# Performance work log

Hardware: AMD Instinct MI355X
Metric: run time of the kernel (lower is better)

## Reference

```python
import jax, jax.numpy as jnp
import numpy as np

TOP_K = 10
RANKING_WEIGHT = 0.3
UP_WEIGHT = 1.0
DOWN_WEIGHT = 0.5
NEG = 1e9  # finite stand-in for -inf so softmax/grads stay NaN-free


def setup_inputs() -> dict:
    key = jax.random.key(0)
    k1, k2, k3, k4 = jax.random.split(key, 4)
    B, N = 1024, 5000
    up_logits = jax.random.normal(k1, (B, N), jnp.float32)
    down_logits = jax.random.normal(k2, (B, N), jnp.float32)
    y_true = jax.random.normal(k3, (B, N), jnp.float32) * 0.05  # daily returns
    masks = jax.random.randint(k4, (B, N), 0, 2).astype(jnp.int32)
    return {"up_logits": up_logits, "down_logits": down_logits,
            "y_true": y_true, "masks": masks}


def _bce_with_logits(x, z):
    # softplus(x) - x*z  ==  -[z*log(sig(x)) + (1-z)*log(1-sig(x))]
    return jax.nn.softplus(x) - x * z


def reference(up_logits, down_logits, y_true, masks):
    maskb = masks > 0                                   # [B, N]
    maskf = maskb.astype(up_logits.dtype)
    num_valid = maskf.sum(-1)                           # [B]
    nv_safe = jnp.maximum(num_valid, 1.0)
    k = jnp.minimum(TOP_K, num_valid.astype(jnp.int32))  # [B] min(top_k, num)

    # Descending rank of y_true among valid entries (invalid pushed to bottom).
    y_desc = jnp.where(maskb, y_true, -NEG)
    rank_desc = jnp.argsort(jnp.argsort(-y_desc, axis=-1), axis=-1)  # [B, N]
    up_labels = (rank_desc < k[:, None]).astype(up_logits.dtype)

    # Ascending rank (biggest losers) for down path.
    y_asc = jnp.where(maskb, y_true, NEG)
    rank_asc = jnp.argsort(jnp.argsort(y_asc, axis=-1), axis=-1)
    down_labels = (rank_asc < k[:, None]).astype(down_logits.dtype)

    # Mean BCE over valid entries per row.
    up_loss = jnp.sum(_bce_with_logits(up_logits, up_labels) * maskf, -1) / nv_safe
    down_loss = jnp.sum(_bce_with_logits(down_logits, down_labels) * maskf, -1) / nv_safe

    # Listwise KL: softmax over valid entries; kl_div(log p, q, 'batchmean')
    # with 1D input of size num divides the sum by num.
    logp = jax.nn.log_softmax(jnp.where(maskb, up_logits, -NEG), axis=-1)
    logq = jax.nn.log_softmax(jnp.where(maskb, y_true, -NEG), axis=-1)
    q = jnp.exp(logq)
    kl = jnp.sum(jnp.where(maskb, q * (logq - logp), 0.0), -1) / nv_safe

    batch_loss = UP_WEIGHT * up_loss + DOWN_WEIGHT * down_loss + RANKING_WEIGHT * kl
    batch_loss = jnp.where(num_valid > 0, batch_loss, 0.0)  # skip empty rows
    return jnp.sum(batch_loss) / up_logits.shape[0]
```

## Files before the change

kernel.cpp:

```cpp
#include <hip/hip_runtime.h>
#include <math.h>

#define NCOLS 5000
#define NF4   1250
#define BLOCK 256
#define NWAVES (BLOCK / 64)
#define NITER 5
#define TOPKK 10
#define TR    3
#define CAP 128

__device__ __forceinline__ unsigned mono_f32(float f) {
  unsigned u = __float_as_uint(f);
  return (u & 0x80000000u) ? ~u : (u | 0x80000000u);
}

__device__ __forceinline__ float wave_sum_f(float v) {
#pragma unroll
  for (int o = 1; o < 64; o <<= 1) v += __shfl_xor(v, o);
  return v;
}
__device__ __forceinline__ int wave_sum_i(int v) {
#pragma unroll
  for (int o = 1; o < 64; o <<= 1) v += __shfl_xor(v, o);
  return v;
}
__device__ __forceinline__ unsigned wave_max_u(unsigned v) {
#pragma unroll
  for (int o = 1; o < 64; o <<= 1) {
    unsigned w = __shfl_xor(v, o);
    v = w > v ? w : v;
  }
  return v;
}

extern "C" __global__ __launch_bounds__(BLOCK, 4)
void row_loss_kernel(const float* __restrict__ up, const float* __restrict__ down,
                     const float* __restrict__ yt, const int* __restrict__ masks,
                     float* __restrict__ ws, float* __restrict__ out,
                     float inv_nrows, int use_ws) {
  __shared__ uint4 km_s[NITER * BLOCK];
  __shared__ float red_f[6][NWAVES];
  __shared__ int red_i[NWAVES];
  __shared__ unsigned t1w_t[NWAVES];
  __shared__ unsigned t1w_b[NWAVES];
  __shared__ unsigned keys_t[CAP];
  __shared__ int      col_t[CAP];
  __shared__ unsigned keys_b[CAP];
  __shared__ int      col_b[CAP];
  __shared__ int ct, cb;
  __shared__ float s_res[2];

  const int tid = threadIdx.x;
  const int lane = tid & 63;
  const int wv = tid >> 6;
  const int row = blockIdx.x;
  const long long b4 = (long long)row * NF4;
  const long long base = (long long)row * NCOLS;

  const float4* up4 = (const float4*)up + b4;
  const float4* dn4 = (const float4*)down + b4;
  const float4* yt4 = (const float4*)yt + b4;
  const int4*   mk4 = (const int4*)masks + b4;

  if (tid == 0) { ct = 0; cb = 0; }

  float4 y4[NITER], u4[NITER], d4[NITER];
  int4 m4[NITER];
#pragma unroll
  for (int j = 0; j < NITER; ++j) {
    const int f = j * BLOCK + tid;
    const int fc = f < NF4 ? f : NF4 - 1;
    y4[j] = yt4[fc];
    u4[j] = up4[fc];
    d4[j] = dn4[fc];
    m4[j] = mk4[fc];
  }
  __builtin_amdgcn_sched_barrier(0);

  int nv_l = 0;
  float sq = 0.f, sp = 0.f, seyy = 0.f, seyu = 0.f, aspu = 0.f, aspd = 0.f;
  unsigned tmax = 0u, tbmax = 0u;
#pragma unroll
  for (int j = 0; j < NITER; ++j) {
    const bool inb = (j * BLOCK + tid) < NF4;
    const float* yp = (const float*)&y4[j];
    const float* upp = (const float*)&u4[j];
    const float* dp = (const float*)&d4[j];
    const int* mp = (const int*)&m4[j];
    unsigned kk[4];
#pragma unroll
    for (int c = 0; c < 4; ++c) {
      const bool valid = inb && (mp[c] > 0);
      const float y = yp[c], u = upp[c], d = dp[c];
      const unsigned kd = valid ? mono_f32(y) : 0u;
      const unsigned kb = valid ? ~kd : 0u;
      kk[c] = kd;
      tmax = kd > tmax ? kd : tmax;
      tbmax = kb > tbmax ? kb : tbmax;
      if (valid) {
        nv_l++;
        const float ey = __expf(y);
        const float eu = __expf(u);
        const float ed = __expf(d);
        sq += ey;
        seyy += ey * y;
        seyu += ey * u;
        sp += eu;
        aspu += (u > 15.f) ? u : __logf(1.f + eu);
        aspd += (d > 15.f) ? d : __logf(1.f + ed);
      }
    }
    km_s[j * BLOCK + tid] = make_uint4(kk[0], kk[1], kk[2], kk[3]);
  }

  nv_l = wave_sum_i(nv_l);
  sq = wave_sum_f(sq);
  sp = wave_sum_f(sp);
  seyy = wave_sum_f(seyy);
  seyu = wave_sum_f(seyu);
  aspu = wave_sum_f(aspu);
  aspd = wave_sum_f(aspd);
  if (lane == 0) {
    red_i[wv] = nv_l;
    red_f[0][wv] = sq;  red_f[1][wv] = sp;
    red_f[2][wv] = seyy; red_f[3][wv] = seyu;
    red_f[4][wv] = aspu; red_f[5][wv] = aspd;
  }

  {
    unsigned vt = tmax, vb = tbmax, t1t = 0u, t1b = 0u;
#pragma unroll
    for (int r = 0; r < TR; ++r) {
      unsigned mt = wave_max_u(vt);
      unsigned mb = wave_max_u(vb);
      if (vt == mt) vt = 0u;
      if (vb == mb) vb = 0u;
      t1t = mt; t1b = mb;
    }
    if (lane == 0) { t1w_t[wv] = t1t; t1w_b[wv] = t1b; }
  }
  __syncthreads();

  int nv = 0;
#pragma unroll
  for (int w = 0; w < NWAVES; ++w) nv += red_i[w];
  const int k = nv < TOPKK ? nv : TOPKK;

  unsigned t1 = 0xFFFFFFFFu, t1b = 0xFFFFFFFFu;
#pragma unroll
  for (int w = 0; w < NWAVES; ++w) {
    t1 = t1w_t[w] < t1 ? t1w_t[w] : t1;
    t1b = t1w_b[w] < t1b ? t1w_b[w] : t1b;
  }

#pragma unroll
  for (int j = 0; j < NITER; ++j) {
    const uint4 kk4 = km_s[j * BLOCK + tid];
    const unsigned ka[4] = {kk4.x, kk4.y, kk4.z, kk4.w};
#pragma unroll
    for (int c = 0; c < 4; ++c) {
      const unsigned kd = ka[c];
      if (kd != 0u) {
        const int col = ((j * BLOCK + tid) << 2) + c;
        if (kd >= t1) {
          int i = atomicAdd(&ct, 1);
          if (i < CAP) { keys_t[i] = kd; col_t[i] = col; }
        }
        const unsigned kb = ~kd;
        if (kb >= t1b) {
          int i = atomicAdd(&cb, 1);
          if (i < CAP) { keys_b[i] = kb; col_b[i] = col; }
        }
      }
    }
  }
  __syncthreads();

  if (wv == 0) {
    const int n = ct < CAP ? ct : CAP;
    const unsigned k0 = (lane < n) ? keys_t[lane] : 0u;
    const unsigned k1 = (64 + lane < n) ? keys_t[64 + lane] : 0u;
    unsigned thr = 0u;
#pragma unroll
    for (int b = 31; b >= 0; --b) {
      const unsigned t = thr | (1u << b);
      const int c = __popcll(__ballot(k0 >= t)) + __popcll(__ballot(k1 >= t));
      thr = (c >= k) ? t : thr;
    }
    float su = 0.f;
    if (k0 >= thr && k0 != 0u) su += up[base + col_t[lane]];
    if (k1 >= thr && k1 != 0u) su += up[base + col_t[64 + lane]];
    su = wave_sum_f(su);
    if (lane == 0) s_res[0] = su;
  } else if (wv == 1) {
    const int n = cb < CAP ? cb : CAP;
    const unsigned k0 = (lane < n) ? keys_b[lane] : 0u;
    const unsigned k1 = (64 + lane < n) ? keys_b[64 + lane] : 0u;
    unsigned thr = 0u;
#pragma unroll
    for (int b = 31; b >= 0; --b) {
      const unsigned t = thr | (1u << b);
      const int c = __popcll(__ballot(k0 >= t)) + __popcll(__ballot(k1 >= t));
      thr = (c >= k) ? t : thr;
    }
    float sd = 0.f;
    if (k0 >= thr && k0 != 0u) sd += down[base + col_b[lane]];
    if (k1 >= thr && k1 != 0u) sd += down[base + col_b[64 + lane]];
    sd = wave_sum_f(sd);
    if (lane == 0) s_res[1] = sd;
  }
  __syncthreads();

  if (tid == 0) {
    float loss = 0.f;
    if (nv > 0) {
      float SQ = 0.f, SP = 0.f, SYY = 0.f, SYU = 0.f, ASU = 0.f, ASD = 0.f;
#pragma unroll
      for (int w = 0; w < NWAVES; ++w) {
        SQ += red_f[0][w]; SP += red_f[1][w];
        SYY += red_f[2][w]; SYU += red_f[3][w];
        ASU += red_f[4][w]; ASD += red_f[5][w];
      }
      const float SU = s_res[0];
      const float SD = s_res[1];
      const float kl = (SYY - SYU) / SQ - __logf(SQ) + __logf(SP);
      const float up_loss = ASU - SU;
      const float dn_loss = ASD - SD;
      loss = (up_loss + 0.5f * dn_loss + 0.3f * kl) / (float)nv;
    }
    if (use_ws) {
      ws[row] = loss;
    } else if (loss != 0.f) {
      atomicAdd(out, loss * inv_nrows);
    }
  }
}

extern "C" __global__ __launch_bounds__(256)
void reduce_loss_kernel(const float* __restrict__ ws, float* __restrict__ out,
                        int n, float inv_n) {
  __shared__ float part[4];
  const int tid = threadIdx.x;
  const int lane = tid & 63;
  const int wv = tid >> 6;
  float s = 0.f;
  const int n4 = n >> 2;
  const float4* w4 = (const float4*)ws;
  for (int i = tid; i < n4; i += 256) {
    const float4 v = w4[i];
    s += (v.x + v.y) + (v.z + v.w);
  }
  for (int i = (n4 << 2) + tid; i < n; i += 256) s += ws[i];
  s = wave_sum_f(s);
  if (lane == 0) part[wv] = s;
  __syncthreads();
  if (tid == 0) out[0] = (part[0] + part[1] + part[2] + part[3]) * inv_n;
}

extern "C" void kernel_launch(void* const* d_in, const int* in_sizes, int n_in,
                              void* d_out, int out_size, void* d_ws, size_t ws_size,
                              hipStream_t stream) {
  const float* up_logits   = (const float*)d_in[0];
  const float* down_logits = (const float*)d_in[1];
  const float* y_true      = (const float*)d_in[2];
  const int*   masks       = (const int*)d_in[3];

  const int nrows = in_sizes[0] / NCOLS;
  const int use_ws = (d_ws != nullptr && ws_size >= (size_t)nrows * sizeof(float)) ? 1 : 0;

  hipMemsetAsync(d_out, 0, sizeof(float) * (size_t)out_size, stream);
  row_loss_kernel<<<nrows, BLOCK, 0, stream>>>(up_logits, down_logits, y_true,
                                               masks, (float*)d_ws, (float*)d_out,
                                               1.0f / (float)nrows, use_ws);
  if (use_ws) {
    reduce_loss_kernel<<<1, 256, 0, stream>>>((const float*)d_ws, (float*)d_out,
                                              nrows, 1.0f / (float)nrows);
  }
}
```

Measured before the change: 115.3 us.

## Use 1024-thread blocks per row with single-max wave thresholds and unconditional workspace reduction

Each row is now processed by a 1024-thread block, so each thread loads at most two float4 chunks per input instead of five. The goal is more memory-level parallelism and less per-thread serial work. The top-3 per-wave threshold search becomes a single per-wave max, with the minimum taken over 16 waves and zero-valued waves ignored. Candidate capacity grows to 256 to absorb the looser threshold. The memset and atomic fallback path are removed, so the two-kernel workspace reduction always runs; this assumes the workspace is always provided.

```diff
diff --git a/kernel.cpp b/kernel.cpp
--- a/kernel.cpp
+++ b/kernel.cpp
@@ -3,12 +3,11 @@
 
 #define NCOLS 5000
 #define NF4   1250
-#define BLOCK 256
-#define NWAVES (BLOCK / 64)
-#define NITER 5
+#define BLOCK 1024
+#define NWAVES 16
+#define T2    (NF4 - BLOCK)
 #define TOPKK 10
-#define TR    3
-#define CAP 128
+#define CAP   256
 
 __device__ __forceinline__ unsigned mono_f32(float f) {
   unsigned u = __float_as_uint(f);
@@ -34,20 +33,17 @@
   return v;
 }
 
-extern "C" __global__ __launch_bounds__(BLOCK, 4)
+extern "C" __global__ __launch_bounds__(BLOCK, 8)
 void row_loss_kernel(const float* __restrict__ up, const float* __restrict__ down,
                      const float* __restrict__ yt, const int* __restrict__ masks,
-                     float* __restrict__ ws, float* __restrict__ out,
-                     float inv_nrows, int use_ws) {
-  __shared__ uint4 km_s[NITER * BLOCK];
+                     float* __restrict__ ws) {
+  __shared__ uint4 km_s[NF4];
   __shared__ float red_f[6][NWAVES];
   __shared__ int red_i[NWAVES];
   __shared__ unsigned t1w_t[NWAVES];
   __shared__ unsigned t1w_b[NWAVES];
-  __shared__ unsigned keys_t[CAP];
-  __shared__ int      col_t[CAP];
-  __shared__ unsigned keys_b[CAP];
-  __shared__ int      col_b[CAP];
+  __shared__ unsigned keys_t[CAP]; __shared__ int col_t[CAP];
+  __shared__ unsigned keys_b[CAP]; __shared__ int col_b[CAP];
   __shared__ int ct, cb;
   __shared__ float s_res[2];
 
@@ -58,61 +54,58 @@
   const long long b4 = (long long)row * NF4;
   const long long base = (long long)row * NCOLS;
 
+  if (tid == 0) { ct = 0; cb = 0; }
+
   const float4* up4 = (const float4*)up + b4;
   const float4* dn4 = (const float4*)down + b4;
   const float4* yt4 = (const float4*)yt + b4;
   const int4*   mk4 = (const int4*)masks + b4;
 
-  if (tid == 0) { ct = 0; cb = 0; }
-
-  float4 y4[NITER], u4[NITER], d4[NITER];
-  int4 m4[NITER];
-#pragma unroll
-  for (int j = 0; j < NITER; ++j) {
-    const int f = j * BLOCK + tid;
-    const int fc = f < NF4 ? f : NF4 - 1;
-    y4[j] = yt4[fc];
-    u4[j] = up4[fc];
-    d4[j] = dn4[fc];
-    m4[j] = mk4[fc];
-  }
+  const bool inb2 = tid < T2;
+  const int f2 = inb2 ? BLOCK + tid : NF4 - 1;
+
+  float4 y0 = yt4[tid], u0 = up4[tid], d0 = dn4[tid];
+  int4   m0 = mk4[tid];
+  float4 y1 = yt4[f2],  u1 = up4[f2],  d1 = dn4[f2];
+  int4   m1 = mk4[f2];
   __builtin_amdgcn_sched_barrier(0);
 
   int nv_l = 0;
   float sq = 0.f, sp = 0.f, seyy = 0.f, seyu = 0.f, aspu = 0.f, aspd = 0.f;
   unsigned tmax = 0u, tbmax = 0u;
-#pragma unroll
-  for (int j = 0; j < NITER; ++j) {
-    const bool inb = (j * BLOCK + tid) < NF4;
-    const float* yp = (const float*)&y4[j];
-    const float* upp = (const float*)&u4[j];
-    const float* dp = (const float*)&d4[j];
-    const int* mp = (const int*)&m4[j];
-    unsigned kk[4];
-#pragma unroll
-    for (int c = 0; c < 4; ++c) {
-      const bool valid = inb && (mp[c] > 0);
-      const float y = yp[c], u = upp[c], d = dp[c];
-      const unsigned kd = valid ? mono_f32(y) : 0u;
-      const unsigned kb = valid ? ~kd : 0u;
-      kk[c] = kd;
-      tmax = kd > tmax ? kd : tmax;
-      tbmax = kb > tbmax ? kb : tbmax;
-      if (valid) {
-        nv_l++;
-        const float ey = __expf(y);
-        const float eu = __expf(u);
-        const float ed = __expf(d);
-        sq += ey;
-        seyy += ey * y;
-        seyu += ey * u;
-        sp += eu;
-        aspu += (u > 15.f) ? u : __logf(1.f + eu);
-        aspd += (d > 15.f) ? d : __logf(1.f + ed);
-      }
-    }
-    km_s[j * BLOCK + tid] = make_uint4(kk[0], kk[1], kk[2], kk[3]);
-  }
+  unsigned kk[4];
+
+#define ELEM(idx, Y, U, D, M, INB)                                      \
+  {                                                                     \
+    const bool valid = (INB) && ((M) > 0);                              \
+    const float y = (Y), u = (U), d = (D);                              \
+    const unsigned kd = valid ? mono_f32(y) : 0u;                       \
+    const unsigned kb = valid ? ~kd : 0u;                               \
+    kk[idx] = kd;                                                       \
+    tmax = kd > tmax ? kd : tmax;                                       \
+    tbmax = kb > tbmax ? kb : tbmax;                                    \
+    if (valid) {                                                        \
+      nv_l++;                                                           \
+      const float ey = __expf(y);                                      \
+      const float eu = __expf(u);                                      \
+      const float ed = __expf(d);                                      \
+      sq += ey; seyy += ey * y; seyu += ey * u; sp += eu;               \
+      aspu += (u > 15.f) ? u : __logf(1.f + eu);                       \
+      aspd += (d > 15.f) ? d : __logf(1.f + ed);                       \
+    }                                                                   \
+  }
+
+  ELEM(0, y0.x, u0.x, d0.x, m0.x, true)
+  ELEM(1, y0.y, u0.y, d0.y, m0.y, true)
+  ELEM(2, y0.z, u0.z, d0.z, m0.z, true)
+  ELEM(3, y0.w, u0.w, d0.w, m0.w, true)
+  km_s[tid] = make_uint4(kk[0], kk[1], kk[2], kk[3]);
+  ELEM(0, y1.x, u1.x, d1.x, m1.x, inb2)
+  ELEM(1, y1.y, u1.y, d1.y, m1.y, inb2)
+  ELEM(2, y1.z, u1.z, d1.z, m1.z, inb2)
+  ELEM(3, y1.w, u1.w, d1.w, m1.w, inb2)
+  if (inb2) km_s[BLOCK + tid] = make_uint4(kk[0], kk[1], kk[2], kk[3]);
+#undef ELEM
 
   nv_l = wave_sum_i(nv_l);
   sq = wave_sum_f(sq);
@@ -121,24 +114,15 @@
   seyu = wave_sum_f(seyu);
   aspu = wave_sum_f(aspu);
   aspd = wave_sum_f(aspd);
+  const unsigned wmax_t = wave_max_u(tmax);
+  const unsigned wmax_b = wave_max_u(tbmax);
   if (lane == 0) {
     red_i[wv] = nv_l;
     red_f[0][wv] = sq;  red_f[1][wv] = sp;
     red_f[2][wv] = seyy; red_f[3][wv] = seyu;
     red_f[4][wv] = aspu; red_f[5][wv] = aspd;
-  }
-
-  {
-    unsigned vt = tmax, vb = tbmax, t1t = 0u, t1b = 0u;
-#pragma unroll
-    for (int r = 0; r < TR; ++r) {
-      unsigned mt = wave_max_u(vt);
-      unsigned mb = wave_max_u(vb);
-      if (vt == mt) vt = 0u;
-      if (vb == mb) vb = 0u;
-      t1t = mt; t1b = mb;
-    }
-    if (lane == 0) { t1w_t[wv] = t1t; t1w_b[wv] = t1b; }
+    t1w_t[wv] = wmax_t;
+    t1w_b[wv] = wmax_b;
   }
   __syncthreads();
 
@@ -150,27 +134,45 @@
   unsigned t1 = 0xFFFFFFFFu, t1b = 0xFFFFFFFFu;
 #pragma unroll
   for (int w = 0; w < NWAVES; ++w) {
-    t1 = t1w_t[w] < t1 ? t1w_t[w] : t1;
-    t1b = t1w_b[w] < t1b ? t1w_b[w] : t1b;
-  }
-
-#pragma unroll
-  for (int j = 0; j < NITER; ++j) {
-    const uint4 kk4 = km_s[j * BLOCK + tid];
-    const unsigned ka[4] = {kk4.x, kk4.y, kk4.z, kk4.w};
+    const unsigned a = t1w_t[w], b = t1w_b[w];
+    if (a != 0u && a < t1) t1 = a;
+    if (b != 0u && b < t1b) t1b = b;
+  }
+
+  {
+    const uint4 c0 = km_s[tid];
+    const unsigned ka[4] = {c0.x, c0.y, c0.z, c0.w};
 #pragma unroll
     for (int c = 0; c < 4; ++c) {
       const unsigned kd = ka[c];
       if (kd != 0u) {
-        const int col = ((j * BLOCK + tid) << 2) + c;
         if (kd >= t1) {
           int i = atomicAdd(&ct, 1);
-          if (i < CAP) { keys_t[i] = kd; col_t[i] = col; }
+          if (i < CAP) { keys_t[i] = kd; col_t[i] = (tid << 2) + c; }
         }
         const unsigned kb = ~kd;
         if (kb >= t1b) {
           int i = atomicAdd(&cb, 1);
-          if (i < CAP) { keys_b[i] = kb; col_b[i] = col; }
+          if (i < CAP) { keys_b[i] = kb; col_b[i] = (tid << 2) + c; }
+        }
+      }
+    }
+  }
+  if (inb2) {
+    const uint4 c1 = km_s[BLOCK + tid];
+    const unsigned ka[4] = {c1.x, c1.y, c1.z, c1.w};
+#pragma unroll
+    for (int c = 0; c < 4; ++c) {
+      const unsigned kd = ka[c];
+      if (kd != 0u) {
+        if (kd >= t1) {
+          int i = atomicAdd(&ct, 1);
+          if (i < CAP) { keys_t[i] = kd; col_t[i] = ((BLOCK + tid) << 2) + c; }
+        }
+        const unsigned kb = ~kd;
+        if (kb >= t1b) {
+          int i = atomicAdd(&cb, 1);
+          if (i < CAP) { keys_b[i] = kb; col_b[i] = ((BLOCK + tid) << 2) + c; }
         }
       }
     }
@@ -179,34 +181,44 @@
 
   if (wv == 0) {
     const int n = ct < CAP ? ct : CAP;
-    const unsigned k0 = (lane < n) ? keys_t[lane] : 0u;
-    const unsigned k1 = (64 + lane < n) ? keys_t[64 + lane] : 0u;
+    unsigned kc[4];
+#pragma unroll
+    for (int t = 0; t < 4; ++t)
+      kc[t] = (t * 64 + lane < n) ? keys_t[t * 64 + lane] : 0u;
     unsigned thr = 0u;
 #pragma unroll
     for (int b = 31; b >= 0; --b) {
       const unsigned t = thr | (1u << b);
-      const int c = __popcll(__ballot(k0 >= t)) + __popcll(__ballot(k1 >= t));
+      int c = 0;
+#pragma unroll
+      for (int q = 0; q < 4; ++q) c += __popcll(__ballot(kc[q] >= t));
       thr = (c >= k) ? t : thr;
     }
     float su = 0.f;
-    if (k0 >= thr && k0 != 0u) su += up[base + col_t[lane]];
-    if (k1 >= thr && k1 != 0u) su += up[base + col_t[64 + lane]];
+#pragma unroll
+    for (int t = 0; t < 4; ++t)
+      if (kc[t] >= thr && kc[t] != 0u) su += up[base + col_t[t * 64 + lane]];
     su = wave_sum_f(su);
     if (lane == 0) s_res[0] = su;
   } else if (wv == 1) {
     const int n = cb < CAP ? cb : CAP;
-    const unsigned k0 = (lane < n) ? keys_b[lane] : 0u;
-    const unsigned k1 = (64 + lane < n) ? keys_b[64 + lane] : 0u;
+    unsigned kc[4];
+#pragma unroll
+    for (int t = 0; t < 4; ++t)
+      kc[t] = (t * 64 + lane < n) ? keys_b[t * 64 + lane] : 0u;
     unsigned thr = 0u;
 #pragma unroll
     for (int b = 31; b >= 0; --b) {
       const unsigned t = thr | (1u << b);
-      const int c = __popcll(__ballot(k0 >= t)) + __popcll(__ballot(k1 >= t));
+      int c = 0;
+#pragma unroll
+      for (int q = 0; q < 4; ++q) c += __popcll(__ballot(kc[q] >= t));
       thr = (c >= k) ? t : thr;
     }
     float sd = 0.f;
-    if (k0 >= thr && k0 != 0u) sd += down[base + col_b[lane]];
-    if (k1 >= thr && k1 != 0u) sd += down[base + col_b[64 + lane]];
+#pragma unroll
+    for (int t = 0; t < 4; ++t)
+      if (kc[t] >= thr && kc[t] != 0u) sd += down[base + col_b[t * 64 + lane]];
     sd = wave_sum_f(sd);
     if (lane == 0) s_res[1] = sd;
   }
@@ -229,11 +241,7 @@
       const float dn_loss = ASD - SD;
       loss = (up_loss + 0.5f * dn_loss + 0.3f * kl) / (float)nv;
     }
-    if (use_ws) {
-      ws[row] = loss;
-    } else if (loss != 0.f) {
-      atomicAdd(out, loss * inv_nrows);
-    }
+    ws[row] = loss;
   }
 }
 
@@ -267,14 +275,9 @@
   const int*   masks       = (const int*)d_in[3];
 
   const int nrows = in_sizes[0] / NCOLS;
-  const int use_ws = (d_ws != nullptr && ws_size >= (size_t)nrows * sizeof(float)) ? 1 : 0;
-
-  hipMemsetAsync(d_out, 0, sizeof(float) * (size_t)out_size, stream);
+
   row_loss_kernel<<<nrows, BLOCK, 0, stream>>>(up_logits, down_logits, y_true,
-                                               masks, (float*)d_ws, (float*)d_out,
-                                               1.0f / (float)nrows, use_ws);
-  if (use_ws) {
-    reduce_loss_kernel<<<1, 256, 0, stream>>>((const float*)d_ws, (float*)d_out,
-                                              nrows, 1.0f / (float)nrows);
-  }
-}
+                                               masks, (float*)d_ws);
+  reduce_loss_kernel<<<1, 256, 0, stream>>>((const float*)d_ws, (float*)d_out,
+                                            nrows, 1.0f / (float)nrows);
+}
```

Measured after the change: 119.0 us. 1.03x slower.

## Stream row data into LDS via async global_load_lds with staged waits

Applied to the files above, without the earlier changes.

Loads y_true, up and down rows straight into shared memory using the async global-to-LDS load builtin, and processes each chunk as soon as its loads land, using explicit vmcnt waits. The stored key array is replaced by a per-thread valid bitmask, and keys are recomputed from LDS. The final top-k gather now reads LDS instead of global memory. The atomic/memset fallback path is dropped and the reduce kernel always runs. The cost is much larger LDS use (about 60KB, launch bounds lowered to 2), which reduces occupancy, and correctness depends on hand-counted vmcnt values.

```diff
diff --git a/kernel.cpp b/kernel.cpp
--- a/kernel.cpp
+++ b/kernel.cpp
@@ -3,12 +3,13 @@
 
 #define NCOLS 5000
 #define NF4   1250
+#define NF4P  1280
 #define BLOCK 256
-#define NWAVES (BLOCK / 64)
+#define NWAVES 4
 #define NITER 5
 #define TOPKK 10
 #define TR    3
-#define CAP 128
+#define CAP   128
 
 __device__ __forceinline__ unsigned mono_f32(float f) {
   unsigned u = __float_as_uint(f);
@@ -34,20 +35,25 @@
   return v;
 }
 
-extern "C" __global__ __launch_bounds__(BLOCK, 4)
+__device__ __forceinline__ void gl_lds16(const float4* g, float4* l) {
+  __builtin_amdgcn_global_load_lds(
+      (const __attribute__((address_space(1))) void*)(g),
+      (__attribute__((address_space(3))) void*)(l), 16, 0, 0);
+}
+
+extern "C" __global__ __launch_bounds__(BLOCK, 2)
 void row_loss_kernel(const float* __restrict__ up, const float* __restrict__ down,
                      const float* __restrict__ yt, const int* __restrict__ masks,
-                     float* __restrict__ ws, float* __restrict__ out,
-                     float inv_nrows, int use_ws) {
-  __shared__ uint4 km_s[NITER * BLOCK];
+                     float* __restrict__ ws) {
+  __shared__ float4 y_s[NF4P];
+  __shared__ float4 u_s[NF4P];
+  __shared__ float4 d_s[NF4P];
   __shared__ float red_f[6][NWAVES];
   __shared__ int red_i[NWAVES];
   __shared__ unsigned t1w_t[NWAVES];
   __shared__ unsigned t1w_b[NWAVES];
-  __shared__ unsigned keys_t[CAP];
-  __shared__ int      col_t[CAP];
-  __shared__ unsigned keys_b[CAP];
-  __shared__ int      col_b[CAP];
+  __shared__ unsigned keys_t[CAP]; __shared__ int col_t[CAP];
+  __shared__ unsigned keys_b[CAP]; __shared__ int col_b[CAP];
   __shared__ int ct, cb;
   __shared__ float s_res[2];
 
@@ -56,65 +62,87 @@
   const int wv = tid >> 6;
   const int row = blockIdx.x;
   const long long b4 = (long long)row * NF4;
-  const long long base = (long long)row * NCOLS;
+
+  if (tid == 0) { ct = 0; cb = 0; }
 
   const float4* up4 = (const float4*)up + b4;
   const float4* dn4 = (const float4*)down + b4;
   const float4* yt4 = (const float4*)yt + b4;
   const int4*   mk4 = (const int4*)masks + b4;
 
-  if (tid == 0) { ct = 0; cb = 0; }
-
-  float4 y4[NITER], u4[NITER], d4[NITER];
   int4 m4[NITER];
 #pragma unroll
   for (int j = 0; j < NITER; ++j) {
     const int f = j * BLOCK + tid;
     const int fc = f < NF4 ? f : NF4 - 1;
-    y4[j] = yt4[fc];
-    u4[j] = up4[fc];
-    d4[j] = dn4[fc];
     m4[j] = mk4[fc];
   }
+
+  {
+    const int wb = wv * 64;
+#pragma unroll
+    for (int j = 0; j < NITER; ++j) {
+      const int f = j * BLOCK + wb + lane;
+      const int fc = f < NF4 ? f : NF4 - 1;
+      gl_lds16(yt4 + fc, y_s + j * BLOCK + wb);
+    }
+#pragma unroll
+    for (int j = 0; j < NITER; ++j) {
+      const int f = j * BLOCK + wb + lane;
+      const int fc = f < NF4 ? f : NF4 - 1;
+      gl_lds16(up4 + fc, u_s + j * BLOCK + wb);
+      gl_lds16(dn4 + fc, d_s + j * BLOCK + wb);
+    }
+  }
   __builtin_amdgcn_sched_barrier(0);
 
-  int nv_l = 0;
+  int vmask = 0;
   float sq = 0.f, sp = 0.f, seyy = 0.f, seyu = 0.f, aspu = 0.f, aspd = 0.f;
   unsigned tmax = 0u, tbmax = 0u;
-#pragma unroll
-  for (int j = 0; j < NITER; ++j) {
-    const bool inb = (j * BLOCK + tid) < NF4;
-    const float* yp = (const float*)&y4[j];
-    const float* upp = (const float*)&u4[j];
-    const float* dp = (const float*)&d4[j];
-    const int* mp = (const int*)&m4[j];
-    unsigned kk[4];
-#pragma unroll
-    for (int c = 0; c < 4; ++c) {
-      const bool valid = inb && (mp[c] > 0);
-      const float y = yp[c], u = upp[c], d = dp[c];
-      const unsigned kd = valid ? mono_f32(y) : 0u;
-      const unsigned kb = valid ? ~kd : 0u;
-      kk[c] = kd;
-      tmax = kd > tmax ? kd : tmax;
-      tbmax = kb > tbmax ? kb : tbmax;
-      if (valid) {
-        nv_l++;
-        const float ey = __expf(y);
-        const float eu = __expf(u);
-        const float ed = __expf(d);
-        sq += ey;
-        seyy += ey * y;
-        seyu += ey * u;
-        sp += eu;
-        aspu += (u > 15.f) ? u : __logf(1.f + eu);
-        aspd += (d > 15.f) ? d : __logf(1.f + ed);
-      }
-    }
-    km_s[j * BLOCK + tid] = make_uint4(kk[0], kk[1], kk[2], kk[3]);
-  }
-
-  nv_l = wave_sum_i(nv_l);
+
+#define ELEM(bit, Y, U, D, M, INB)                                      \
+  {                                                                     \
+    const bool valid = (INB) && ((M) > 0);                              \
+    const float y = (Y), u = (U), d = (D);                              \
+    const unsigned kd = valid ? mono_f32(y) : 0u;                       \
+    const unsigned kb = valid ? ~kd : 0u;                               \
+    vmask |= valid ? (1 << (bit)) : 0;                                  \
+    tmax = kd > tmax ? kd : tmax;                                       \
+    tbmax = kb > tbmax ? kb : tbmax;                                    \
+    if (valid) {                                                        \
+      const float ey = __expf(y);                                       \
+      const float eu = __expf(u);                                       \
+      const float ed = __expf(d);                                       \
+      sq += ey; seyy += ey * y; seyu += ey * u; sp += eu;               \
+      aspu += (u > 15.f) ? u : __logf(1.f + eu);                        \
+      aspd += (d > 15.f) ? d : __logf(1.f + ed);                        \
+    }                                                                   \
+  }
+
+#define CHUNK(J, VM, INB)                                               \
+  {                                                                     \
+    asm volatile("s_waitcnt vmcnt(" VM ")" ::: "memory");               \
+    __builtin_amdgcn_sched_barrier(0);                                  \
+    const float4 yv = y_s[(J) * BLOCK + tid];                           \
+    const float4 uv = u_s[(J) * BLOCK + tid];                           \
+    const float4 dv = d_s[(J) * BLOCK + tid];                           \
+    const int4 mm = m4[(J)];                                            \
+    ELEM((J) * 4 + 0, yv.x, uv.x, dv.x, mm.x, INB)                      \
+    ELEM((J) * 4 + 1, yv.y, uv.y, dv.y, mm.y, INB)                      \
+    ELEM((J) * 4 + 2, yv.z, uv.z, dv.z, mm.z, INB)                      \
+    ELEM((J) * 4 + 3, yv.w, uv.w, dv.w, mm.w, INB)                      \
+  }
+
+  const bool inb2 = tid < (NF4 - 4 * BLOCK);
+  CHUNK(0, "8", true)
+  CHUNK(1, "6", true)
+  CHUNK(2, "4", true)
+  CHUNK(3, "2", true)
+  CHUNK(4, "0", inb2)
+#undef CHUNK
+#undef ELEM
+
+  int nv_l = wave_sum_i(__popc((unsigned)vmask));
   sq = wave_sum_f(sq);
   sp = wave_sum_f(sp);
   seyy = wave_sum_f(seyy);
@@ -129,16 +157,16 @@
   }
 
   {
-    unsigned vt = tmax, vb = tbmax, t1t = 0u, t1b = 0u;
+    unsigned vt = tmax, vb = tbmax, t1t = 0u, t1b_ = 0u;
 #pragma unroll
     for (int r = 0; r < TR; ++r) {
       unsigned mt = wave_max_u(vt);
       unsigned mb = wave_max_u(vb);
       if (vt == mt) vt = 0u;
       if (vb == mb) vb = 0u;
-      t1t = mt; t1b = mb;
-    }
-    if (lane == 0) { t1w_t[wv] = t1t; t1w_b[wv] = t1b; }
+      t1t = mt; t1b_ = mb;
+    }
+    if (lane == 0) { t1w_t[wv] = t1t; t1w_b[wv] = t1b_; }
   }
   __syncthreads();
 
@@ -156,21 +184,24 @@
 
 #pragma unroll
   for (int j = 0; j < NITER; ++j) {
-    const uint4 kk4 = km_s[j * BLOCK + tid];
-    const unsigned ka[4] = {kk4.x, kk4.y, kk4.z, kk4.w};
-#pragma unroll
-    for (int c = 0; c < 4; ++c) {
-      const unsigned kd = ka[c];
-      if (kd != 0u) {
-        const int col = ((j * BLOCK + tid) << 2) + c;
-        if (kd >= t1) {
-          int i = atomicAdd(&ct, 1);
-          if (i < CAP) { keys_t[i] = kd; col_t[i] = col; }
-        }
-        const unsigned kb = ~kd;
-        if (kb >= t1b) {
-          int i = atomicAdd(&cb, 1);
-          if (i < CAP) { keys_b[i] = kb; col_b[i] = col; }
+    const int mbits = (vmask >> (j * 4)) & 0xF;
+    if (mbits) {
+      const float4 yv = y_s[j * BLOCK + tid];
+      const float ya[4] = {yv.x, yv.y, yv.z, yv.w};
+#pragma unroll
+      for (int c = 0; c < 4; ++c) {
+        if (mbits & (1 << c)) {
+          const unsigned kd = mono_f32(ya[c]);
+          const int col = ((j * BLOCK + tid) << 2) + c;
+          if (kd >= t1) {
+            int i = atomicAdd(&ct, 1);
+            if (i < CAP) { keys_t[i] = kd; col_t[i] = col; }
+          }
+          const unsigned kb = ~kd;
+          if (kb >= t1b) {
+            int i = atomicAdd(&cb, 1);
+            if (i < CAP) { keys_b[i] = kb; col_b[i] = col; }
+          }
         }
       }
     }
@@ -189,8 +220,8 @@
       thr = (c >= k) ? t : thr;
     }
     float su = 0.f;
-    if (k0 >= thr && k0 != 0u) su += up[base + col_t[lane]];
-    if (k1 >= thr && k1 != 0u) su += up[base + col_t[64 + lane]];
+    if (k0 >= thr && k0 != 0u) su += ((const float*)u_s)[col_t[lane]];
+    if (k1 >= thr && k1 != 0u) su += ((const float*)u_s)[col_t[64 + lane]];
     su = wave_sum_f(su);
     if (lane == 0) s_res[0] = su;
   } else if (wv == 1) {
@@ -205,8 +236,8 @@
       thr = (c >= k) ? t : thr;
     }
     float sd = 0.f;
-    if (k0 >= thr && k0 != 0u) sd += down[base + col_b[lane]];
-    if (k1 >= thr && k1 != 0u) sd += down[base + col_b[64 + lane]];
+    if (k0 >= thr && k0 != 0u) sd += ((const float*)d_s)[col_b[lane]];
+    if (k1 >= thr && k1 != 0u) sd += ((const float*)d_s)[col_b[64 + lane]];
     sd = wave_sum_f(sd);
     if (lane == 0) s_res[1] = sd;
   }
@@ -229,11 +260,7 @@
       const float dn_loss = ASD - SD;
       loss = (up_loss + 0.5f * dn_loss + 0.3f * kl) / (float)nv;
     }
-    if (use_ws) {
-      ws[row] = loss;
-    } else if (loss != 0.f) {
-      atomicAdd(out, loss * inv_nrows);
-    }
+    ws[row] = loss;
   }
 }
 
@@ -267,14 +294,9 @@
   const int*   masks       = (const int*)d_in[3];
 
   const int nrows = in_sizes[0] / NCOLS;
-  const int use_ws = (d_ws != nullptr && ws_size >= (size_t)nrows * sizeof(float)) ? 1 : 0;
-
-  hipMemsetAsync(d_out, 0, sizeof(float) * (size_t)out_size, stream);
+
   row_loss_kernel<<<nrows, BLOCK, 0, stream>>>(up_logits, down_logits, y_true,
-                                               masks, (float*)d_ws, (float*)d_out,
-                                               1.0f / (float)nrows, use_ws);
-  if (use_ws) {
-    reduce_loss_kernel<<<1, 256, 0, stream>>>((const float*)d_ws, (float*)d_out,
-                                              nrows, 1.0f / (float)nrows);
-  }
-}
+                                               masks, (float*)d_ws);
+  reduce_loss_kernel<<<1, 256, 0, stream>>>((const float*)d_ws, (float*)d_out,
+                                            nrows, 1.0f / (float)nrows);
+}
```

Measured after the change: 122.4 us. 1.06x slower.
